# Performance work log

Hardware: AMD Instinct MI355X
Metric: run time of the kernel (lower is better)

The kernel has to match this reference:

```python
import jax, jax.numpy as jnp
import numpy as np

HEADS = 16
DIM_HEAD = 128
DIM = HEADS * DIM_HEAD          # hidden_size = 2048
SEGMENT_LEN = 496
NUM_LONGTERM = 16
NUM_PERSIST = 16
C = SEGMENT_LEN + NUM_LONGTERM  # total_segment_len = 512 (window width)
EPS = 1e-6
THETA = 10000.0
NEG = -jnp.finfo(jnp.float32).max


def _rope(t, cos, sin):
    # t: [b, h, n, d]; cos/sin: [n, d]; interleaved (rotate-half on adjacent pairs)
    t2 = t.reshape(t.shape[:-1] + (DIM_HEAD // 2, 2))
    rot = jnp.stack((-t2[..., 1], t2[..., 0]), axis=-1).reshape(t.shape)
    return t * cos + rot * sin


def _attn_bias():
    # queries: [m_len longterm-mem tokens | segment tokens]
    # keys:    [p_len persistent | m_len longterm-mem | segment tokens]
    q_len = C
    k_len = C + NUM_PERSIST
    pq = NUM_LONGTERM
    pk = NUM_PERSIST + NUM_LONGTERM
    bias = jnp.full((q_len, k_len), NEG, dtype=jnp.float32)
    bias = bias.at[:, :pk].set(0.0)  # everyone attends to the prefix
    sq = q_len - pq
    causal = jnp.tril(jnp.ones((sq, sq), dtype=bool))
    bias = bias.at[pq:, pk:].set(jnp.where(causal, 0.0, NEG))
    return bias


def setup_inputs() -> dict:
    key = jax.random.key(0)
    k1, k2, k3, k4 = jax.random.split(key, 4)
    b, n = 2, 4096  # n must be a multiple of C=512
    return {
        "x": jax.random.normal(k1, (b, n, DIM), dtype=jnp.float32),
        "norm_w": jnp.ones((DIM,), dtype=jnp.float32),
        "w_qkv": jax.random.normal(k2, (3 * DIM, DIM), dtype=jnp.float32) * 0.02,
        "w_out": jax.random.normal(k3, (DIM, DIM), dtype=jnp.float32) * 0.02,
        "pm": jax.random.normal(k4, (2, HEADS, NUM_PERSIST, DIM_HEAD), dtype=jnp.float32) * 0.02,
    }


def reference(x, norm_w, w_qkv, w_out, pm):
    b, n, d = x.shape
    # RMSNorm
    xn = x * jax.lax.rsqrt(jnp.mean(x * x, axis=-1, keepdims=True) + EPS) * norm_w
    # qkv projection (Linear, no bias)
    qkv = xn @ w_qkv.T
    q, k, v = jnp.split(qkv, 3, axis=-1)

    def to_heads(t):  # [b, n, h*d] -> [b, h, n, d]
        return t.reshape(b, n, HEADS, DIM_HEAD).transpose(0, 2, 1, 3)

    q, k, v = to_heads(q), to_heads(k), to_heads(v)

    # RoPE over full sequence positions 0..n-1 (before windowing)
    inv_freq = 1.0 / (THETA ** (jnp.arange(0, DIM_HEAD, 2, dtype=jnp.float32) / DIM_HEAD))
    freqs = jnp.arange(n, dtype=jnp.float32)[:, None] * inv_freq  # [n, d/2]
    freqs = jnp.repeat(freqs, 2, axis=-1)                          # [n, d]
    cos, sin = jnp.cos(freqs), jnp.sin(freqs)
    q = _rope(q, cos, sin)
    k = _rope(k, cos, sin)

    # split into windows of width C: [b, h, n, d] -> [(b*w), h, C, d]
    w = n // C

    def to_windows(t):
        return t.reshape(b, HEADS, w, C, DIM_HEAD).transpose(0, 2, 1, 3, 4).reshape(b * w, HEADS, C, DIM_HEAD)

    q, k, v = to_windows(q), to_windows(k), to_windows(v)

    # prepend persistent memory tokens to k, v
    pmk = jnp.broadcast_to(pm[0], (b * w, HEADS, NUM_PERSIST, DIM_HEAD))
    pmv = jnp.broadcast_to(pm[1], (b * w, HEADS, NUM_PERSIST, DIM_HEAD))
    k = jnp.concatenate((pmk, k), axis=-2)  # [(b*w), h, C+P, d]
    v = jnp.concatenate((pmv, v), axis=-2)

    bias = _attn_bias()  # [C, C+P]
    scale = DIM_HEAD ** -0.5
    sim = jnp.einsum('whqd,whkd->whqk', q, k) * scale + bias
    attn = jax.nn.softmax(sim, axis=-1)
    out = jnp.einsum('whqk,whkd->whqd', attn, v)

    # '(b w) h c d -> b (w c) (h d)'
    out = out.reshape(b, w, HEADS, C, DIM_HEAD).transpose(0, 1, 3, 2, 4).reshape(b, n, HEADS * DIM_HEAD)
    return out @ w_out.T
```

## Files before the change

kernel.cpp:

```cpp
#include <hip/hip_runtime.h>
#include <hip/hip_bf16.h>

typedef __attribute__((ext_vector_type(8))) short short8v;
typedef __attribute__((ext_vector_type(4))) float f32x4;
typedef __attribute__((ext_vector_type(4))) unsigned short us4;
typedef __attribute__((ext_vector_type(4))) unsigned u32x4;

#define DEV static __device__ __forceinline__

DEV unsigned short f2bf(float f) {
  unsigned u = __builtin_bit_cast(unsigned, f);
  u += 0x7FFFu + ((u >> 16) & 1u);
  return (unsigned short)(u >> 16);
}
DEV float bf2f(unsigned short s) {
  unsigned u = ((unsigned)s) << 16;
  return __builtin_bit_cast(float, u);
}
DEV void gload16(const void* g, void* l) {
  __builtin_amdgcn_global_load_lds((const __attribute__((address_space(1))) void*)g,
                                   (__attribute__((address_space(3))) void*)l, 16, 0, 0);
}

__global__ __launch_bounds__(256) void k_prep(const float* __restrict__ w_qkv,
                                              unsigned short* __restrict__ wqkvb,
                                              const float* __restrict__ w_out,
                                              unsigned short* __restrict__ woutb,
                                              const float* __restrict__ pm,
                                              unsigned short* __restrict__ pmk,
                                              unsigned short* __restrict__ vt,
                                              unsigned short* __restrict__ zbuf,
                                              float* __restrict__ ct,
                                              float* __restrict__ st,
                                              const float* __restrict__ x,
                                              const float* __restrict__ norm_w,
                                              unsigned short* __restrict__ xb) {
  __shared__ float red[4];
  const int b = blockIdx.x, tid = threadIdx.x;
  if (b < 12288) {
    long i = (long)b * 256 + tid;
    f32x4 v = *((const f32x4*)w_qkv + i);
    us4 o;
    o[0] = f2bf(v[0]); o[1] = f2bf(v[1]); o[2] = f2bf(v[2]); o[3] = f2bf(v[3]);
    *((us4*)wqkvb + i) = o;
  } else if (b < 16384) {
    long i = (long)(b - 12288) * 256 + tid;
    f32x4 v = *((const f32x4*)w_out + i);
    us4 o;
    o[0] = f2bf(v[0]); o[1] = f2bf(v[1]); o[2] = f2bf(v[2]); o[3] = f2bf(v[3]);
    *((us4*)woutb + i) = o;
  } else if (b < 16512) {
    int idx = (b - 16384) * 256 + tid;
    if (idx < 8) zbuf[idx] = 0;
    int d = idx & 127, p = (idx >> 7) & 15, h = idx >> 11;
    float kvl = pm[((0 * 16 + h) * 16 + p) * 128 + d];
    float vvl = pm[((1 * 16 + h) * 16 + p) * 128 + d];
    pmk[(h * 16 + p) * 128 + d] = f2bf(kvl);
    unsigned short vb = f2bf(vvl);
    for (int w = 0; w < 16; ++w) {
      long base = ((long)(w * 16 + h) * 128 + d) * 576;
      vt[base + p] = vb;
      vt[base + 528 + p] = 0;
      vt[base + 544 + p] = 0;
      vt[base + 560 + p] = 0;
    }
  } else if (b < 17536) {
    int idx = (b - 16512) * 256 + tid;
    int pos = idx >> 6, i = idx & 63;
    float invf = __powf(10000.f, -(float)i * (1.f / 64.f));
    float a = (float)pos * invf;
    ct[idx] = cosf(a);
    st[idx] = sinf(a);
  } else {
    int row = b - 17536;
    const f32x4* xr = (const f32x4*)(x + (long)row * 2048);
    f32x4 v0 = xr[tid * 2], v1 = xr[tid * 2 + 1];
    float ss = v0[0]*v0[0] + v0[1]*v0[1] + v0[2]*v0[2] + v0[3]*v0[3]
             + v1[0]*v1[0] + v1[1]*v1[1] + v1[2]*v1[2] + v1[3]*v1[3];
    ss += __shfl_xor(ss, 1);  ss += __shfl_xor(ss, 2);  ss += __shfl_xor(ss, 4);
    ss += __shfl_xor(ss, 8);  ss += __shfl_xor(ss, 16); ss += __shfl_xor(ss, 32);
    if ((tid & 63) == 0) red[tid >> 6] = ss;
    __syncthreads();
    float tot = red[0] + red[1] + red[2] + red[3];
    float rs = rsqrtf(tot * (1.f / 2048.f) + 1e-6f);
    float xv[8] = {v0[0], v0[1], v0[2], v0[3], v1[0], v1[1], v1[2], v1[3]};
    short8v pack;
#pragma unroll
    for (int j = 0; j < 8; ++j) pack[j] = (short)f2bf(xv[j] * rs * norm_w[tid * 8 + j]);
    *((short8v*)(xb + (long)row * 2048) + tid) = pack;
  }
}


#define VMCNT4 asm volatile("s_waitcnt vmcnt(4)" ::: "memory")
#define VMCNT0 asm volatile("s_waitcnt vmcnt(0)" ::: "memory")
#define SCHEDB __builtin_amdgcn_sched_barrier(0)
#define NOSTG ((void)0)

template <int OUTF32>
__global__ __launch_bounds__(512, 2) void k_gemm8(const unsigned short* __restrict__ A,
                                                  const unsigned short* __restrict__ B,
                                                  unsigned short* __restrict__ Cb,
                                                  float* __restrict__ Cf,
                                                  int M, int N, int K) {
  __shared__ __align__(16) unsigned short lds[4 * 256 * 64];
  const int tid = threadIdx.x;
  const int lane = tid & 63;
  const int ql = lane & 15, g = lane >> 4;
  const int wid = tid >> 6;
  const int wm = wid >> 2, wn = wid & 3;

  const int nbx = N >> 8;
  const int nwg = gridDim.x;
  int bid = blockIdx.x;
  int swz = (bid & 7) * (nwg >> 3) + (bid >> 3);
  int by = swz / nbx, bx = swz - by * nbx;
  const long rowA0 = (long)by << 8;
  const long rowB0 = (long)bx << 8;

  const int idx0 = tid, idx1 = 512 + tid;
  const int dr0 = idx0 >> 3, sc0 = (idx0 & 7) ^ (dr0 & 7);
  const int dr1 = idx1 >> 3, sc1 = (idx1 & 7) ^ (dr1 & 7);
  const long halfA = 128L * K;
  const unsigned short* pA0 = A + (rowA0 + dr0) * (long)K + sc0 * 8;
  const unsigned short* pA1 = A + (rowA0 + dr1) * (long)K + sc1 * 8;
  const unsigned short* pB0 = B + (rowB0 + dr0) * (long)K + sc0 * 8;
  const unsigned short* pB1 = B + (rowB0 + dr1) * (long)K + sc1 * 8;

  const int rsw0 = (g ^ (ql & 7)) * 8;
  const int rsw1 = ((4 + g) ^ (ql & 7)) * 8;

  short8v fa[4], fb[2][4];
  f32x4 acc[8][4] = {};

#define STAGE_A(b, h, kk) do { \
  gload16(pA0 + (long)(h) * halfA + (kk), lds + (b) * 32768 + (h) * 8192 + (idx0 << 3)); \
  gload16(pA1 + (long)(h) * halfA + (kk), lds + (b) * 32768 + (h) * 8192 + (idx1 << 3)); } while (0)
#define STAGE_B(b, h, kk) do { \
  gload16(pB0 + (long)(h) * halfA + (kk), lds + (b) * 32768 + 16384 + (h) * 8192 + (idx0 << 3)); \
  gload16(pB1 + (long)(h) * halfA + (kk), lds + (b) * 32768 + 16384 + (h) * 8192 + (idx1 << 3)); } while (0)

#define PHASE(buf, mh, ks, LOADB, STG, VMC) do { \
  { const unsigned short* p_ = lds + (buf) * 32768 + (((wm << 7) + (mh) * 64 + ql) << 6) + ((ks) ? rsw1 : rsw0); \
    _Pragma("unroll") for (int mi_ = 0; mi_ < 4; ++mi_) fa[mi_] = *(const short8v*)(p_ + (mi_ << 10)); } \
  if (LOADB) { const unsigned short* p_ = lds + (buf) * 32768 + 16384 + (((wn << 6) + ql) << 6) + ((ks) ? rsw1 : rsw0); \
    _Pragma("unroll") for (int n_ = 0; n_ < 4; ++n_) fb[ks][n_] = *(const short8v*)(p_ + (n_ << 10)); } \
  STG; \
  SCHEDB; __builtin_amdgcn_s_barrier(); SCHEDB; \
  __builtin_amdgcn_s_setprio(1); \
  _Pragma("unroll") for (int mi_ = 0; mi_ < 4; ++mi_) \
    _Pragma("unroll") for (int n_ = 0; n_ < 4; ++n_) \
      acc[(mh) * 4 + mi_][n_] = __builtin_amdgcn_mfma_f32_16x16x32_bf16(fa[mi_], fb[ks][n_], acc[(mh) * 4 + mi_][n_], 0, 0, 0); \
  __builtin_amdgcn_s_setprio(0); \
  VMC; \
  SCHEDB; __builtin_amdgcn_s_barrier(); SCHEDB; \
} while (0)

  const int NT = K >> 6;
  const int NITER = NT >> 1;

  STAGE_A(0, 0, 0); STAGE_A(0, 1, 0);
  STAGE_B(0, 0, 0); STAGE_B(0, 1, 0);
  STAGE_B(1, 0, 64); STAGE_B(1, 1, 64);
  VMCNT4;
  SCHEDB; __builtin_amdgcn_s_barrier(); SCHEDB;

  for (int i = 0; i < NITER - 1; ++i) {
    const int k1 = (2 * i + 1) << 6;
    const int k2 = (2 * i + 2) << 6;
    const int k3 = (2 * i + 3) << 6;
    PHASE(0, 0, 0, 1, STAGE_A(1, 0, k1), NOSTG);
    PHASE(0, 0, 1, 1, STAGE_A(1, 1, k1), NOSTG);
    PHASE(0, 1, 0, 0, STAGE_B(0, 0, k2), NOSTG);
    PHASE(0, 1, 1, 0, STAGE_B(0, 1, k2), VMCNT4);
    PHASE(1, 0, 0, 1, STAGE_A(0, 0, k2), NOSTG);
    PHASE(1, 0, 1, 1, STAGE_A(0, 1, k2), NOSTG);
    PHASE(1, 1, 0, 0, STAGE_B(1, 0, k3), NOSTG);
    PHASE(1, 1, 1, 0, STAGE_B(1, 1, k3), VMCNT4);
  }
  {
    const int k1 = (NT - 1) << 6;
    PHASE(0, 0, 0, 1, STAGE_A(1, 0, k1), NOSTG);
    PHASE(0, 0, 1, 1, STAGE_A(1, 1, k1), NOSTG);
    PHASE(0, 1, 0, 0, NOSTG, NOSTG);
    PHASE(0, 1, 1, 0, NOSTG, VMCNT0);
    PHASE(1, 0, 0, 1, NOSTG, NOSTG);
    PHASE(1, 0, 1, 1, NOSTG, NOSTG);
    PHASE(1, 1, 0, 0, NOSTG, NOSTG);
    PHASE(1, 1, 1, 0, NOSTG, NOSTG);
  }

#pragma unroll
  for (int am = 0; am < 8; ++am)
#pragma unroll
    for (int n = 0; n < 4; ++n)
#pragma unroll
      for (int r = 0; r < 4; ++r) {
        long row = rowA0 + (wm << 7) + am * 16 + (g << 2) + r;
        long col = rowB0 + (wn << 6) + n * 16 + ql;
        if (OUTF32) Cf[row * N + col] = acc[am][n][r];
        else        Cb[row * N + col] = f2bf(acc[am][n][r]);
      }
#undef STAGE_A
#undef STAGE_B
#undef PHASE
}

__global__ __launch_bounds__(256) void k_kprep(unsigned short* __restrict__ qkv,
                                               unsigned short* __restrict__ vt,
                                               const float* __restrict__ ct,
                                               const float* __restrict__ st) {
  __shared__ unsigned short lt[64 * 136];
  const int tile = blockIdx.x, h = blockIdx.y;
  const int tid = threadIdx.x;
  const int t0 = tile * 64;
  {
    int row = t0 + (tid >> 2);
    int d0 = (tid & 3) * 32;
    int pos = row & 4095;
    unsigned short* kp = qkv + (long)row * 6144 + 2048 + h * 128 + d0;
    const float* cp = ct + pos * 64 + (d0 >> 1);
    const float* sp = st + pos * 64 + (d0 >> 1);
    f32x4 cv[4], sv[4];
#pragma unroll
    for (int j = 0; j < 4; ++j) { cv[j] = *(const f32x4*)(cp + j * 4); sv[j] = *(const f32x4*)(sp + j * 4); }
    short8v kv[4];
#pragma unroll
    for (int j = 0; j < 4; ++j) kv[j] = *(const short8v*)(kp + j * 8);
#pragma unroll
    for (int j = 0; j < 4; ++j) {
      short8v outv;
#pragma unroll
      for (int p = 0; p < 4; ++p) {
        float a = bf2f((unsigned short)kv[j][2 * p]);
        float b = bf2f((unsigned short)kv[j][2 * p + 1]);
        float c = cv[j][p], s = sv[j][p];
        outv[2 * p]     = (short)f2bf(a * c - b * s);
        outv[2 * p + 1] = (short)f2bf(b * c + a * s);
      }
      *(short8v*)(kp + j * 8) = outv;
    }
  }
  {
    int row = tid >> 2, seg = tid & 3;
    const unsigned short* src = qkv + (long)(t0 + row) * 6144 + 4096 + h * 128 + seg * 32;
#pragma unroll
    for (int j = 0; j < 4; ++j)
      *(short8v*)(lt + row * 136 + seg * 32 + j * 8) = *(const short8v*)(src + j * 8);
  }
  __syncthreads();
  int d = tid >> 1, half = tid & 1;
  int wh = t0 >> 9;
  long dst = ((long)(wh * 16 + h) * 128 + d) * 576 + (t0 & 511) + 16 + half * 32;
  unsigned short tmp[32];
#pragma unroll
  for (int kk = 0; kk < 32; ++kk) tmp[kk] = lt[(half * 32 + kk) * 136 + d];
#pragma unroll
  for (int j = 0; j < 4; ++j) {
    short8v v;
#pragma unroll
    for (int e = 0; e < 8; ++e) v[e] = (short)tmp[j * 8 + e];
    *(short8v*)(vt + dst + j * 8) = v;
  }
}

__global__ __launch_bounds__(512) void k_attn(const unsigned short* __restrict__ qkv,
                                              const unsigned short* __restrict__ vt,
                                              const unsigned short* __restrict__ pmk,
                                              const unsigned short* __restrict__ zbuf,
                                              const float* __restrict__ ct,
                                              const float* __restrict__ stt,
                                              unsigned short* __restrict__ attno) {
  __shared__ __align__(16) unsigned short Ks[2][32 * 128];
  __shared__ __align__(16) unsigned short Vs[2][128 * 32];
  __shared__ unsigned Ps[8][16][16];
  const int wh = blockIdx.x, h = blockIdx.y, qb = blockIdx.z;
  const int tid = threadIdx.x;
  const int wave = tid >> 6, lane = tid & 63;
  const int ql = lane & 15, g = lane >> 4;
  const int tokbase = (wh >> 3) * 4096 + (wh & 7) * 512;
  const int qi = qb * 128 + wave * 16 + ql;
  const int wqmin = qb * 128 + wave * 16;
  const int wqmax = wqmin + 15;
  const long qrow = (long)(tokbase + qi) * 6144;
  const int pos = (tokbase + qi) & 4095;
  short8v qf[4];
#pragma unroll
  for (int ks = 0; ks < 4; ++ks) {
    short8v qv = *(const short8v*)(qkv + qrow + h * 128 + ks * 32 + g * 8);
    f32x4 cv = *(const f32x4*)(ct + pos * 64 + ks * 16 + g * 4);
    f32x4 sv = *(const f32x4*)(stt + pos * 64 + ks * 16 + g * 4);
    const float SC = 0.08838834764831845f;
#pragma unroll
    for (int p = 0; p < 4; ++p) {
      float a = bf2f((unsigned short)qv[2 * p]);
      float b = bf2f((unsigned short)qv[2 * p + 1]);
      qf[ks][2 * p]     = (short)f2bf((a * cv[p] - b * sv[p]) * SC);
      qf[ks][2 * p + 1] = (short)f2bf((b * cv[p] + a * sv[p]) * SC);
    }
  }
  const int nkt = min(17, (qb * 128 + 144 + 31) >> 5);
  const long vbase = (long)(wh * 16 + h) * 128 * 576;

  float mrun = -3.0e38f, lrun = 0.f;
  f32x4 o[8] = {};

#define STAGEKV(kt, b) do { \
    { int kl_ = tid >> 4, dc_ = tid & 15, dcs_ = dc_ ^ (kl_ & 7); \
      int ki_ = (kt) * 32 + kl_; \
      const unsigned short* src_; \
      if (ki_ < 16)       src_ = pmk + (h * 16 + ki_) * 128 + dcs_ * 8; \
      else if (ki_ < 528) src_ = qkv + (long)(tokbase + ki_ - 16) * 6144 + 2048 + h * 128 + dcs_ * 8; \
      else                src_ = zbuf; \
      gload16(src_, &Ks[b][0] + (size_t)tid * 8); } \
    { int d_ = tid >> 2, kc_ = tid & 3, kcs_ = kc_ ^ (d_ & 3); \
      gload16(vt + vbase + (long)d_ * 576 + (kt) * 32 + kcs_ * 8, &Vs[b][0] + (size_t)tid * 8); } \
  } while (0)

  STAGEKV(0, 0);
  __syncthreads();
  for (int kt = 0; kt < nkt; ++kt) {
    const int cur = kt & 1;
    if (kt + 1 < nkt) STAGEKV(kt + 1, cur ^ 1);
    if (kt * 32 <= wqmax + 16) {
      f32x4 stv[2] = {};
      __builtin_amdgcn_s_setprio(1);
#pragma unroll
      for (int kf = 0; kf < 2; ++kf) {
        int row = kf * 16 + ql;
#pragma unroll
        for (int ks = 0; ks < 4; ++ks) {
          int chunk = (ks * 4 + g) ^ (row & 7);
          short8v kv = *(const short8v*)(&Ks[cur][0] + row * 128 + chunk * 8);
          stv[kf] = __builtin_amdgcn_mfma_f32_16x16x32_bf16(kv, qf[ks], stv[kf], 0, 0, 0);
        }
      }
      __builtin_amdgcn_s_setprio(0);
      float tmax = -3.0e38f;
      const bool needmask = !(kt == 0 || (kt * 32 + 15 <= wqmin));
      if (needmask) {
#pragma unroll
        for (int kf = 0; kf < 2; ++kf)
#pragma unroll
          for (int r = 0; r < 4; ++r) {
            int ki = kt * 32 + kf * 16 + g * 4 + r;
            bool ok = (ki < 32) || (qi >= 16 && ki <= qi + 16);
            float s = ok ? stv[kf][r] : -3.0e38f;
            stv[kf][r] = s;
            tmax = fmaxf(tmax, s);
          }
      } else {
#pragma unroll
        for (int kf = 0; kf < 2; ++kf)
#pragma unroll
          for (int r = 0; r < 4; ++r) tmax = fmaxf(tmax, stv[kf][r]);
      }
      tmax = fmaxf(tmax, __shfl_xor(tmax, 16));
      tmax = fmaxf(tmax, __shfl_xor(tmax, 32));
      if (!__all(tmax <= mrun + 8.f)) {
        float mnew = fmaxf(mrun, tmax);
        float corr = __expf(mrun - mnew);
        lrun *= corr;
#pragma unroll
        for (int db = 0; db < 8; ++db) {
          o[db][0] *= corr; o[db][1] *= corr; o[db][2] *= corr; o[db][3] *= corr;
        }
        mrun = mnew;
      }
      float psum = 0.f;
#pragma unroll
      for (int kf = 0; kf < 2; ++kf)
#pragma unroll
        for (int r = 0; r < 4; ++r) {
          float p = __expf(stv[kf][r] - mrun);
          stv[kf][r] = p;
          psum += p;
        }
      psum += __shfl_xor(psum, 16);
      psum += __shfl_xor(psum, 32);
      lrun += psum;
#pragma unroll
      for (int kf = 0; kf < 2; ++kf) {
        unsigned w01 = (unsigned)f2bf(stv[kf][0]) | ((unsigned)f2bf(stv[kf][1]) << 16);
        unsigned w23 = (unsigned)f2bf(stv[kf][2]) | ((unsigned)f2bf(stv[kf][3]) << 16);
        int pr = kf * 8 + 2 * g;
        Ps[wave][pr][ql ^ (pr & 7)] = w01;
        Ps[wave][pr + 1][ql ^ ((pr + 1) & 7)] = w23;
      }
      u32x4 pbw;
#pragma unroll
      for (int t = 0; t < 4; ++t) {
        int pr = 4 * g + t;
        pbw[t] = Ps[wave][pr][ql ^ (pr & 7)];
      }
      short8v pb = __builtin_bit_cast(short8v, pbw);
      __builtin_amdgcn_s_setprio(1);
#pragma unroll
      for (int db = 0; db < 8; ++db) {
        int d = db * 16 + ql;
        int kc = g ^ (d & 3);
        short8v vf = *(const short8v*)(&Vs[cur][0] + d * 32 + kc * 8);
        o[db] = __builtin_amdgcn_mfma_f32_16x16x32_bf16(vf, pb, o[db], 0, 0, 0);
      }
      __builtin_amdgcn_s_setprio(0);
    }
    __syncthreads();
  }
#undef STAGEKV
  float inv = 1.0f / lrun;
  long obase = (long)(tokbase + qi) * 2048 + h * 128;
#pragma unroll
  for (int db = 0; db < 8; ++db) {
    us4 ov;
#pragma unroll
    for (int r = 0; r < 4; ++r) ov[r] = f2bf(o[db][r] * inv);
    *(us4*)(attno + obase + db * 16 + g * 4) = ov;
  }
}

extern "C" void kernel_launch(void* const* d_in, const int* in_sizes, int n_in,
                              void* d_out, int out_size, void* d_ws, size_t ws_size,
                              hipStream_t stream) {
  const float* x      = (const float*)d_in[0];
  const float* norm_w = (const float*)d_in[1];
  const float* w_qkv  = (const float*)d_in[2];
  const float* w_out  = (const float*)d_in[3];
  const float* pm     = (const float*)d_in[4];
  float* out = (float*)d_out;

  char* ws = (char*)d_ws;
  size_t off = 0;
  auto alloc = [&](size_t bytes) -> void* {
    void* p = ws + off;
    off += (bytes + 255) & ~(size_t)255;
    return p;
  };
  unsigned short* xb    = (unsigned short*)alloc(8192ull * 2048 * 2);
  unsigned short* wqkvb = (unsigned short*)alloc(6144ull * 2048 * 2);
  unsigned short* woutb = (unsigned short*)alloc(2048ull * 2048 * 2);
  unsigned short* qkv   = (unsigned short*)alloc(8192ull * 6144 * 2);
  unsigned short* vt    = (unsigned short*)alloc(256ull * 128 * 576 * 2);
  unsigned short* attno = (unsigned short*)alloc(8192ull * 2048 * 2);
  unsigned short* pmk   = (unsigned short*)alloc(16 * 16 * 128 * 2);
  float* ct             = (float*)alloc(4096 * 64 * 4);
  float* stt            = (float*)alloc(4096 * 64 * 4);
  unsigned short* zbuf  = (unsigned short*)alloc(256);

  hipLaunchKernelGGL(k_prep, dim3(25728), dim3(256), 0, stream,
                     w_qkv, wqkvb, w_out, woutb, pm, pmk, vt, zbuf, ct, stt, x, norm_w, xb);
  hipLaunchKernelGGL((k_gemm8<0>), dim3(24 * 32), dim3(512), 0, stream,
                     xb, wqkvb, qkv, (float*)nullptr, 8192, 6144, 2048);
  hipLaunchKernelGGL(k_kprep, dim3(128, 16), dim3(256), 0, stream, qkv, vt, ct, stt);
  hipLaunchKernelGGL(k_attn, dim3(16, 16, 4), dim3(512), 0, stream,
                     qkv, vt, pmk, zbuf, ct, stt, attno);
  hipLaunchKernelGGL((k_gemm8<1>), dim3(8 * 32), dim3(512), 0, stream,
                     attno, woutb, (unsigned short*)nullptr, out, 8192, 2048, 2048);
}
```

Before: 403.0 us.

## Process two query chunks per attention block to reuse staged K/V tiles

Each attention workgroup now handles two 128-query chunks (queries z*256 and z*256+128) sharing the same double-buffered K/V LDS tiles, halving the grid along z. This is meant to cut redundant global-to-LDS K/V traffic and per-block overhead. The per-tile cross-lane reduction of the softmax denominator is deferred to the epilogue. In exchange it doubles accumulator and Q-fragment registers and reduces the number of blocks, which may lower occupancy and parallelism.

```diff
diff --git a/kernel.cpp b/kernel.cpp
--- a/kernel.cpp
+++ b/kernel.cpp
@@ -274,36 +274,38 @@
   __shared__ __align__(16) unsigned short Ks[2][32 * 128];
   __shared__ __align__(16) unsigned short Vs[2][128 * 32];
   __shared__ unsigned Ps[8][16][16];
-  const int wh = blockIdx.x, h = blockIdx.y, qb = blockIdx.z;
+  const int wh = blockIdx.x, h = blockIdx.y, z = blockIdx.z;
   const int tid = threadIdx.x;
   const int wave = tid >> 6, lane = tid & 63;
   const int ql = lane & 15, g = lane >> 4;
   const int tokbase = (wh >> 3) * 4096 + (wh & 7) * 512;
-  const int qi = qb * 128 + wave * 16 + ql;
-  const int wqmin = qb * 128 + wave * 16;
-  const int wqmax = wqmin + 15;
-  const long qrow = (long)(tokbase + qi) * 6144;
-  const int pos = (tokbase + qi) & 4095;
-  short8v qf[4];
-#pragma unroll
-  for (int ks = 0; ks < 4; ++ks) {
-    short8v qv = *(const short8v*)(qkv + qrow + h * 128 + ks * 32 + g * 8);
-    f32x4 cv = *(const f32x4*)(ct + pos * 64 + ks * 16 + g * 4);
-    f32x4 sv = *(const f32x4*)(stt + pos * 64 + ks * 16 + g * 4);
-    const float SC = 0.08838834764831845f;
-#pragma unroll
-    for (int p = 0; p < 4; ++p) {
-      float a = bf2f((unsigned short)qv[2 * p]);
-      float b = bf2f((unsigned short)qv[2 * p + 1]);
-      qf[ks][2 * p]     = (short)f2bf((a * cv[p] - b * sv[p]) * SC);
-      qf[ks][2 * p + 1] = (short)f2bf((b * cv[p] + a * sv[p]) * SC);
+  const int q0 = z * 256 + wave * 16 + ql;
+  short8v qf[2][4];
+#pragma unroll
+  for (int c = 0; c < 2; ++c) {
+    const int qi = q0 + c * 128;
+    const long qrow = (long)(tokbase + qi) * 6144;
+    const int pos = (tokbase + qi) & 4095;
+#pragma unroll
+    for (int ks = 0; ks < 4; ++ks) {
+      short8v qv = *(const short8v*)(qkv + qrow + h * 128 + ks * 32 + g * 8);
+      f32x4 cv = *(const f32x4*)(ct + pos * 64 + ks * 16 + g * 4);
+      f32x4 sv = *(const f32x4*)(stt + pos * 64 + ks * 16 + g * 4);
+      const float SC = 0.08838834764831845f;
+#pragma unroll
+      for (int p = 0; p < 4; ++p) {
+        float a = bf2f((unsigned short)qv[2 * p]);
+        float b = bf2f((unsigned short)qv[2 * p + 1]);
+        qf[c][ks][2 * p]     = (short)f2bf((a * cv[p] - b * sv[p]) * SC);
+        qf[c][ks][2 * p + 1] = (short)f2bf((b * cv[p] + a * sv[p]) * SC);
+      }
     }
   }
-  const int nkt = min(17, (qb * 128 + 144 + 31) >> 5);
+  const int nkt = min(17, (z * 256 + 256 + 144 + 31) >> 5);
   const long vbase = (long)(wh * 16 + h) * 128 * 576;
 
-  float mrun = -3.0e38f, lrun = 0.f;
-  f32x4 o[8] = {};
+  float mrun[2] = {-3.0e38f, -3.0e38f}, lrun[2] = {0.f, 0.f};
+  f32x4 o[2][8] = {};
 
 #define STAGEKV(kt, b) do { \
     { int kl_ = tid >> 4, dc_ = tid & 15, dcs_ = dc_ ^ (kl_ & 7); \
@@ -322,7 +324,11 @@
   for (int kt = 0; kt < nkt; ++kt) {
     const int cur = kt & 1;
     if (kt + 1 < nkt) STAGEKV(kt + 1, cur ^ 1);
-    if (kt * 32 <= wqmax + 16) {
+#pragma unroll
+    for (int c = 0; c < 2; ++c) {
+      const int qi = q0 + c * 128;
+      const int wqmin = z * 256 + c * 128 + wave * 16;
+      if (kt * 32 > wqmin + 15 + 16) continue;
       f32x4 stv[2] = {};
       __builtin_amdgcn_s_setprio(1);
 #pragma unroll
@@ -332,7 +338,7 @@
         for (int ks = 0; ks < 4; ++ks) {
           int chunk = (ks * 4 + g) ^ (row & 7);
           short8v kv = *(const short8v*)(&Ks[cur][0] + row * 128 + chunk * 8);
-          stv[kf] = __builtin_amdgcn_mfma_f32_16x16x32_bf16(kv, qf[ks], stv[kf], 0, 0, 0);
+          stv[kf] = __builtin_amdgcn_mfma_f32_16x16x32_bf16(kv, qf[c][ks], stv[kf], 0, 0, 0);
         }
       }
       __builtin_amdgcn_s_setprio(0);
@@ -357,28 +363,25 @@
       }
       tmax = fmaxf(tmax, __shfl_xor(tmax, 16));
       tmax = fmaxf(tmax, __shfl_xor(tmax, 32));
-      if (!__all(tmax <= mrun + 8.f)) {
-        float mnew = fmaxf(mrun, tmax);
-        float corr = __expf(mrun - mnew);
-        lrun *= corr;
+      if (!__all(tmax <= mrun[c] + 8.f)) {
+        float mnew = fmaxf(mrun[c], tmax);
+        float corr = __expf(mrun[c] - mnew);
+        lrun[c] *= corr;
 #pragma unroll
         for (int db = 0; db < 8; ++db) {
-          o[db][0] *= corr; o[db][1] *= corr; o[db][2] *= corr; o[db][3] *= corr;
+          o[c][db][0] *= corr; o[c][db][1] *= corr;
+          o[c][db][2] *= corr; o[c][db][3] *= corr;
         }
-        mrun = mnew;
-      }
-      float psum = 0.f;
+        mrun[c] = mnew;
+      }
 #pragma unroll
       for (int kf = 0; kf < 2; ++kf)
 #pragma unroll
         for (int r = 0; r < 4; ++r) {
-          float p = __expf(stv[kf][r] - mrun);
+          float p = __expf(stv[kf][r] - mrun[c]);
           stv[kf][r] = p;
-          psum += p;
+          lrun[c] += p;
         }
-      psum += __shfl_xor(psum, 16);
-      psum += __shfl_xor(psum, 32);
-      lrun += psum;
 #pragma unroll
       for (int kf = 0; kf < 2; ++kf) {
         unsigned w01 = (unsigned)f2bf(stv[kf][0]) | ((unsigned)f2bf(stv[kf][1]) << 16);
@@ -400,21 +403,27 @@
         int d = db * 16 + ql;
         int kc = g ^ (d & 3);
         short8v vf = *(const short8v*)(&Vs[cur][0] + d * 32 + kc * 8);
-        o[db] = __builtin_amdgcn_mfma_f32_16x16x32_bf16(vf, pb, o[db], 0, 0, 0);
+        o[c][db] = __builtin_amdgcn_mfma_f32_16x16x32_bf16(vf, pb, o[c][db], 0, 0, 0);
       }
       __builtin_amdgcn_s_setprio(0);
     }
     __syncthreads();
   }
 #undef STAGEKV
-  float inv = 1.0f / lrun;
-  long obase = (long)(tokbase + qi) * 2048 + h * 128;
-#pragma unroll
-  for (int db = 0; db < 8; ++db) {
-    us4 ov;
-#pragma unroll
-    for (int r = 0; r < 4; ++r) ov[r] = f2bf(o[db][r] * inv);
-    *(us4*)(attno + obase + db * 16 + g * 4) = ov;
+#pragma unroll
+  for (int c = 0; c < 2; ++c) {
+    float l = lrun[c];
+    l += __shfl_xor(l, 16);
+    l += __shfl_xor(l, 32);
+    float inv = 1.0f / l;
+    long obase = (long)(tokbase + q0 + c * 128) * 2048 + h * 128;
+#pragma unroll
+    for (int db = 0; db < 8; ++db) {
+      us4 ov;
+#pragma unroll
+      for (int r = 0; r < 4; ++r) ov[r] = f2bf(o[c][db][r] * inv);
+      *(us4*)(attno + obase + db * 16 + g * 4) = ov;
+    }
   }
 }
 
@@ -451,7 +460,7 @@
   hipLaunchKernelGGL((k_gemm8<0>), dim3(24 * 32), dim3(512), 0, stream,
                      xb, wqkvb, qkv, (float*)nullptr, 8192, 6144, 2048);
   hipLaunchKernelGGL(k_kprep, dim3(128, 16), dim3(256), 0, stream, qkv, vt, ct, stt);
-  hipLaunchKernelGGL(k_attn, dim3(16, 16, 4), dim3(512), 0, stream,
+  hipLaunchKernelGGL(k_attn, dim3(16, 16, 2), dim3(512), 0, stream,
                      qkv, vt, pmk, zbuf, ct, stt, attno);
   hipLaunchKernelGGL((k_gemm8<1>), dim3(8 * 32), dim3(512), 0, stream,
                      attno, woutb, (unsigned short*)nullptr, out, 8192, 2048, 2048);
```

New measurement: 416.0 us. 1.03x slower.
